# Optimization experiments

Hardware: AMD Instinct MI355X
Metric: run time of the kernel (lower is better)

The kernel has to match this reference:

```python
import jax, jax.numpy as jnp
import numpy as np

NIN = 128
NOUT = 128


def setup_inputs() -> dict:
    key = jax.random.key(0)
    k_adj, k_node, k_wi, k_wj = jax.random.split(key, 4)
    B, N = 4, 256
    adj = jax.random.uniform(k_adj, (B, 1, N, N), dtype=jnp.float32)
    node = jax.random.normal(k_node, (B, NIN, N), dtype=jnp.float32)
    # 1x1 conv weights, stored as [nout, nin] (squeezed from [nout, nin, 1, 1])
    scale = 1.0 / np.sqrt(NIN)
    Wi = jax.random.normal(k_wi, (NOUT, NIN), dtype=jnp.float32) * scale
    Wj = jax.random.normal(k_wj, (NOUT, NIN), dtype=jnp.float32) * scale
    return {"adj": adj, "node": node, "Wi": Wi, "Wj": Wj}


def reference(adj, node, Wi, Wj):
    # adj: [B,1,N,N], node: [B,nin,N]
    N = adj.shape[-1]
    # broadcast node across rows and mask by adjacency: [B,nin,N,N]
    x = node[:, :, None, :] * adj
    # 1x1 convs == channel contractions
    yi = jnp.einsum('oc,bcij->boij', Wi, x)
    yj = jnp.einsum('oc,bcij->boij', Wj, x)
    I = jnp.eye(N, dtype=x.dtype)
    return I * yi + (1.0 - I) * yj
```

## Files before the change

### kernel.cpp

```cpp
#include <hip/hip_runtime.h>

#define NIN  128
#define NOUT 128
#define NN   256
#define BB   4

typedef float f4 __attribute__((ext_vector_type(4)));

__global__ __launch_bounds__(1024, 2) void nodeconv_fused(
    const float* __restrict__ adj,
    const float* __restrict__ node,
    const float* __restrict__ Wi,
    const float* __restrict__ Wj,
    float* __restrict__ out)
{
    __shared__ float part[2][2][NN];
    __shared__ float si[NN];
    __shared__ float sj[NN];

    const int bo = blockIdx.x;
    const int b  = bo >> 7;
    const int o  = bo & (NOUT - 1);
    const int t  = threadIdx.x;

    {
        const int j   = t & 255;
        const int sel = (t >> 8) & 1;
        const int h   = t >> 9;
        const float* w   = (sel ? Wj : Wi) + o * NIN + h * 64;
        const float* np_ = node + ((size_t)b * NIN + h * 64) * NN + j;
        float a = 0.f;
        #pragma unroll 16
        for (int c = 0; c < 64; ++c)
            a = fmaf(w[c], np_[(size_t)c * NN], a);
        part[h][sel][j] = a;
    }
    __syncthreads();
    if (t < 512) {
        const int j   = t & 255;
        const int sel = t >> 8;
        const float v = part[0][sel][j] + part[1][sel][j];
        (sel ? sj : si)[j] = v;
    }
    __syncthreads();

    const int jb = (t & 63) << 2;
    const int rr = t >> 6;

    const f4 vj = *(const f4*)&sj[jb];

    const float* adjb = adj + (size_t)b * (NN * NN);
    float*       outp = out + (size_t)bo * (NN * NN);

    const int ibase = rr << 4;
    #pragma unroll 8
    for (int r = 0; r < 16; ++r) {
        const int i = ibase + r;
        const float s_ii = si[i];
        const f4 a = *(const f4*)&adjb[i * NN + jb];
        f4 v;
        v.x = (i == jb + 0) ? s_ii : vj.x;
        v.y = (i == jb + 1) ? s_ii : vj.y;
        v.z = (i == jb + 2) ? s_ii : vj.z;
        v.w = (i == jb + 3) ? s_ii : vj.w;
        f4 rs = a * v;
        __builtin_nontemporal_store(rs, (f4*)&outp[i * NN + jb]);
    }
}

extern "C" void kernel_launch(void* const* d_in, const int* in_sizes, int n_in,
                              void* d_out, int out_size, void* d_ws, size_t ws_size,
                              hipStream_t stream) {
    const float* adj  = (const float*)d_in[0];
    const float* node = (const float*)d_in[1];
    const float* Wi   = (const float*)d_in[2];
    const float* Wj   = (const float*)d_in[3];
    float* out = (float*)d_out;

    nodeconv_fused<<<dim3(BB * NOUT), dim3(1024), 0, stream>>>(adj, node, Wi, Wj, out);
}
```

Baseline: 164.8 us.

## Split each output plane across four smaller blocks with vectorized projection

Replaces the 1024-thread-per-(batch,channel) kernel with 256-thread blocks that each write a quarter of the rows, quadrupling the grid. The channel projection is vectorized with float4 node loads and computes both Wi and Wj accumulators from each load. Each block redundantly recomputes the full projection row, and output stores become regular instead of nontemporal. The aim is better occupancy and latency hiding for the store-bound phase, at the cost of extra projection work and cache traffic.

```diff
diff --git a/kernel.cpp b/kernel.cpp
--- a/kernel.cpp
+++ b/kernel.cpp
@@ -7,64 +7,70 @@
 
 typedef float f4 __attribute__((ext_vector_type(4)));
 
-__global__ __launch_bounds__(1024, 2) void nodeconv_fused(
+__global__ __launch_bounds__(256) void nodeconv_one(
     const float* __restrict__ adj,
     const float* __restrict__ node,
     const float* __restrict__ Wi,
     const float* __restrict__ Wj,
     float* __restrict__ out)
 {
-    __shared__ float part[2][2][NN];
-    __shared__ float si[NN];
-    __shared__ float sj[NN];
+    __shared__ f4    part[2][4][64];
+    __shared__ float su[2][NN];
 
-    const int bo = blockIdx.x;
-    const int b  = bo >> 7;
-    const int o  = bo & (NOUT - 1);
-    const int t  = threadIdx.x;
+    const int blk = blockIdx.x;
+    const int bo  = blk >> 2;
+    const int qc  = blk & 3;
+    const int b   = bo >> 7;
+    const int o   = bo & (NOUT - 1);
+    const int t   = threadIdx.x;
 
     {
-        const int j   = t & 255;
-        const int sel = (t >> 8) & 1;
-        const int h   = t >> 9;
-        const float* w   = (sel ? Wj : Wi) + o * NIN + h * 64;
-        const float* np_ = node + ((size_t)b * NIN + h * 64) * NN + j;
-        float a = 0.f;
-        #pragma unroll 16
-        for (int c = 0; c < 64; ++c)
-            a = fmaf(w[c], np_[(size_t)c * NN], a);
-        part[h][sel][j] = a;
+        const int tq = t & 63;
+        const int g  = t >> 6;
+        const f4*    np4 = (const f4*)node + ((size_t)b * NIN + g * 32) * 64 + tq;
+        const float* wi  = Wi + o * NIN + g * 32;
+        const float* wj  = Wj + o * NIN + g * 32;
+        f4 ai = {0.f, 0.f, 0.f, 0.f};
+        f4 aj = {0.f, 0.f, 0.f, 0.f};
+        #pragma unroll 8
+        for (int c = 0; c < 32; ++c) {
+            const f4 n = np4[(size_t)c * 64];
+            ai += wi[c] * n;
+            aj += wj[c] * n;
+        }
+        part[0][g][tq] = ai;
+        part[1][g][tq] = aj;
     }
     __syncthreads();
-    if (t < 512) {
-        const int j   = t & 255;
-        const int sel = t >> 8;
-        const float v = part[0][sel][j] + part[1][sel][j];
-        (sel ? sj : si)[j] = v;
+    if (t < 128) {
+        const int tq  = t & 63;
+        const int sel = t >> 6;
+        const f4 s = part[sel][0][tq] + part[sel][1][tq]
+                   + part[sel][2][tq] + part[sel][3][tq];
+        *(f4*)&su[sel][tq << 2] = s;
     }
     __syncthreads();
 
     const int jb = (t & 63) << 2;
     const int rr = t >> 6;
 
-    const f4 vj = *(const f4*)&sj[jb];
+    const f4 vj = *(const f4*)&su[1][jb];
 
     const float* adjb = adj + (size_t)b * (NN * NN);
     float*       outp = out + (size_t)bo * (NN * NN);
 
-    const int ibase = rr << 4;
-    #pragma unroll 8
+    const int i0 = (qc << 6) + rr;
+    #pragma unroll
     for (int r = 0; r < 16; ++r) {
-        const int i = ibase + r;
-        const float s_ii = si[i];
+        const int i = i0 + (r << 2);
+        const float s_ii = su[0][i];
         const f4 a = *(const f4*)&adjb[i * NN + jb];
         f4 v;
         v.x = (i == jb + 0) ? s_ii : vj.x;
         v.y = (i == jb + 1) ? s_ii : vj.y;
         v.z = (i == jb + 2) ? s_ii : vj.z;
         v.w = (i == jb + 3) ? s_ii : vj.w;
-        f4 rs = a * v;
-        __builtin_nontemporal_store(rs, (f4*)&outp[i * NN + jb]);
+        *(f4*)&outp[i * NN + jb] = a * v;
     }
 }
 
@@ -77,5 +83,5 @@
     const float* Wj   = (const float*)d_in[3];
     float* out = (float*)d_out;
 
-    nodeconv_fused<<<dim3(BB * NOUT), dim3(1024), 0, stream>>>(adj, node, Wi, Wj, out);
+    nodeconv_one<<<dim3(BB * NOUT * 4), dim3(256), 0, stream>>>(adj, node, Wi, Wj, out);
 }
```

Result: faster. 156.8 us (-4.9%).
